# Kernel optimization log

Measured on AMD Instinct MI355X. Metric: run time of the kernel, lower is better.

The kernel has to match this reference:

```python
import jax, jax.numpy as jnp
import numpy as np
import math

DIM = 1024
NUM_HEADS = 16
HEAD_DIM = DIM // NUM_HEADS
EPS = 1e-6
DILATED = 2
WINDOW = 2  # window_size init arg; actual window = L * WINDOW per side


def setup_inputs() -> dict:
    key = jax.random.key(0)
    ks = jax.random.split(key, 14)
    B, S = 1, 8704
    x = jax.random.normal(ks[0], (B, S, DIM), jnp.float32)
    ang = jax.random.uniform(ks[1], (S, HEAD_DIM // 2), jnp.float32, -jnp.pi, jnp.pi)
    freqs_cos = jnp.cos(ang)
    freqs_sin = jnp.sin(ang)
    def lin(k):
        return 0.02 * jax.random.normal(k, (DIM, DIM), jnp.float32)
    def bias(k):
        return 0.01 * jax.random.normal(k, (DIM,), jnp.float32)
    return {
        'x': x, 'freqs_cos': freqs_cos, 'freqs_sin': freqs_sin,
        'wq': lin(ks[2]), 'bq': bias(ks[3]),
        'wk': lin(ks[4]), 'bk': bias(ks[5]),
        'wv': lin(ks[6]), 'bv': bias(ks[7]),
        'wo': lin(ks[8]), 'bo': bias(ks[9]),
        'gq': 1.0 + 0.02 * jax.random.normal(ks[10], (DIM,), jnp.float32),
        'gk': 1.0 + 0.02 * jax.random.normal(ks[11], (DIM,), jnp.float32),
        'f': 34, 'L': 256,
    }


def rmsnorm(h, g):
    return h * jax.lax.rsqrt(jnp.mean(h * h, axis=-1, keepdims=True) + EPS) * g


def rope(h, cos, sin):
    # h: [B,S,D] viewed as interleaved complex pairs per head, rotated by unit freqs
    B, S, D = h.shape
    hp = h.reshape(B, S, NUM_HEADS, HEAD_DIM // 2, 2)
    a, b = hp[..., 0], hp[..., 1]
    c = cos[None, :, None, :]
    s = sin[None, :, None, :]
    ra = a * c - b * s
    rb = a * s + b * c
    return jnp.stack([ra, rb], axis=-1).reshape(B, S, D)


def windowed_attention(q, k, v, w):
    # sliding-window attention: query i attends keys j with |i-j| <= w (inclusive)
    B, S, D = q.shape
    H, hd = NUM_HEADS, HEAD_DIM
    def heads(t):
        return t.reshape(B, S, H, hd).transpose(0, 2, 1, 3)  # [B,H,S,hd]
    qh, kh, vh = heads(q), heads(k), heads(v)
    C = w  # block size == window -> only 3 neighbor key blocks per query block
    pad = (-S) % C
    Sp = S + pad
    nb = Sp // C
    def blocks(t):
        return jnp.pad(t, ((0, 0), (0, 0), (0, pad), (0, 0))).reshape(B, H, nb, C, hd)
    qb = blocks(qh)
    def win(t):
        tb = jnp.pad(blocks(t), ((0, 0), (0, 0), (1, 1), (0, 0), (0, 0)))
        return jnp.concatenate([tb[:, :, i:i + nb] for i in range(3)], axis=3)  # [B,H,nb,3C,hd]
    kw_, vw_ = win(kh), win(vh)
    scores = jnp.einsum('bhnqd,bhnkd->bhnqk', qb, kw_) * (1.0 / math.sqrt(hd))
    qi = jnp.arange(nb)[:, None, None] * C + jnp.arange(C)[None, :, None]      # [nb,C,1]
    kj = (jnp.arange(nb)[:, None, None] - 1) * C + jnp.arange(3 * C)[None, None, :]  # [nb,1,3C]
    valid = (kj >= 0) & (kj < S) & (qi - kj <= w) & (kj - qi <= w)
    scores = jnp.where(valid, scores, -1e9)
    p = jax.nn.softmax(scores, axis=-1)
    o = jnp.einsum('bhnqk,bhnkd->bhnqd', p, vw_)
    return o.reshape(B, H, Sp, hd)[:, :, :S].transpose(0, 2, 1, 3).reshape(B, S, D)


def reference(x, freqs_cos, freqs_sin, wq, bq, wk, bk, wv, bv, wo, bo, gq, gk, f, L):
    B, S, D = x.shape
    q = rope(rmsnorm(x @ wq + bq, gq), freqs_cos, freqs_sin)
    k = rope(rmsnorm(x @ wk + bk, gk), freqs_cos, freqs_sin)
    v = x @ wv + bv
    w = L * WINDOW
    use_dilated = DILATED > 1 and S // (DILATED * L) > 1
    if use_dilated:
        blk = DILATED * L
        pad_len = blk - S % blk  # == blk when S % blk == 0 (faithful to torch code)
        Sp = S + pad_len
        n = Sp // blk
        def padd(t):
            return jnp.pad(t, ((0, 0), (0, pad_len), (0, 0)))
        def dil(t):
            # 'b (n d l) c -> (b d) (n l) c'
            return t.reshape(B, n, DILATED, L, D).transpose(0, 2, 1, 3, 4).reshape(B * DILATED, n * L, D)
        q, k, v = dil(padd(q)), dil(padd(k)), dil(padd(v))
    o = windowed_attention(q, k, v, w)
    out = o @ wo + bo
    if use_dilated:
        # '(b d) (n l) c -> b (n d l) c', then drop pad
        out = out.reshape(B, DILATED, n, L, D).transpose(0, 2, 1, 3, 4).reshape(B, n * DILATED * L, D)
        out = out[:, :S]
    return out
```

## Files before the change

kernel.cpp:

```cpp
#include <hip/hip_runtime.h>
#include <hip/hip_bf16.h>
#include <stdint.h>

#define DIM 1024
#define NH 16
#define HD 64
#define S_ORIG 8704
#define WIN 512

typedef __attribute__((ext_vector_type(8))) short short8;
typedef __attribute__((ext_vector_type(4))) float f32x4;

__device__ __forceinline__ float bf2f(unsigned short u) {
    return __uint_as_float(((unsigned int)u) << 16);
}
__device__ __forceinline__ unsigned short f2bf(float f) {
    unsigned int x = __float_as_uint(f);
    unsigned int r = x + 0x7fffu + ((x >> 16) & 1u);
    return (unsigned short)(r >> 16);
}
__device__ __forceinline__ unsigned int pkbf(float a, float b) {
    unsigned int ua = (__float_as_uint(a) + 0x8000u) >> 16;
    unsigned int ub = (__float_as_uint(b) + 0x8000u) & 0xffff0000u;
    return ua | ub;
}

#define GLD_LDS(gptr, lptr) \
    __builtin_amdgcn_global_load_lds((const __attribute__((address_space(1))) void*)(gptr), \
                                     (__attribute__((address_space(3))) void*)(lptr), 16, 0, 0)

__global__ __launch_bounds__(256) void cvt_x(const float* __restrict__ x,
                                             unsigned short* __restrict__ xb) {
    int i = (blockIdx.x * 256 + threadIdx.x) * 4;
    float4 v = *(const float4*)(x + i);
    ushort4 o;
    o.x = f2bf(v.x); o.y = f2bf(v.y); o.z = f2bf(v.z); o.w = f2bf(v.w);
    *(ushort4*)(xb + i) = o;
}

__global__ __launch_bounds__(256) void transpose_w(const float* __restrict__ w0,
                                                   const float* __restrict__ w1,
                                                   const float* __restrict__ w2,
                                                   const float* __restrict__ w3,
                                                   unsigned short* __restrict__ wt) {
    __shared__ float ts[64][65];
    const int z = blockIdx.z;
    const float* w = z == 0 ? w0 : z == 1 ? w1 : z == 2 ? w2 : w3;
    unsigned short* o = wt + (size_t)z * DIM * DIM;
    const int kb = blockIdx.x * 64, nb = blockIdx.y * 64;
    const int t = threadIdx.x, c = t & 63, r4 = t >> 6;
#pragma unroll
    for (int rr = 0; rr < 16; rr++) {
        int row = rr * 4 + r4;
        ts[row][c] = w[(size_t)(kb + row) * DIM + nb + c];
    }
    __syncthreads();
#pragma unroll
    for (int rr = 0; rr < 16; rr++) {
        int nl = rr * 4 + r4;
        o[(size_t)(nb + nl) * DIM + kb + c] = f2bf(ts[c][nl]);
    }
}

template <int OUTF32>
__global__ __launch_bounds__(256) void gemm_bf16(const unsigned short* __restrict__ A,
                                                 const unsigned short* __restrict__ Bt,
                                                 const float* __restrict__ b0,
                                                 const float* __restrict__ b1,
                                                 const float* __restrict__ b2,
                                                 void* __restrict__ Cout) {
    __shared__ __align__(16) unsigned short As[128 * 32];
    __shared__ __align__(16) unsigned short Bs[128 * 32];
    const int z = blockIdx.z;
    const unsigned short* B = Bt + (size_t)z * DIM * DIM;
    const float* bias = z == 0 ? b0 : (z == 1 ? b1 : b2);
    const int m0 = blockIdx.y * 128, n0 = blockIdx.x * 128;
    const int tid = threadIdx.x;
    const int lane = tid & 63, wv = tid >> 6;
    const int wr = wv >> 1, wc = wv & 1;
    const int quad = lane >> 4, r = lane & 15;

    f32x4 acc[4][4];
#pragma unroll
    for (int i = 0; i < 4; i++)
#pragma unroll
        for (int j = 0; j < 4; j++)
#pragma unroll
            for (int t4 = 0; t4 < 4; t4++) acc[i][j][t4] = 0.0f;

    const unsigned short* a_base = A + (size_t)m0 * DIM;
    const unsigned short* b_base = B + (size_t)n0 * DIM;
    const int c0 = wv * 128 + lane;
    const int r0 = c0 >> 2, o0 = (c0 & 3) * 8;
    const int c1 = c0 + 64;
    const int r1 = c1 >> 2, o1 = (c1 & 3) * 8;
    unsigned short* lA0 = &As[(size_t)(wv * 128) * 8];
    unsigned short* lA1 = &As[(size_t)(wv * 128 + 64) * 8];
    unsigned short* lB0 = &Bs[(size_t)(wv * 128) * 8];
    unsigned short* lB1 = &Bs[(size_t)(wv * 128 + 64) * 8];

    for (int k0 = 0; k0 < DIM; k0 += 32) {
        __syncthreads();
        GLD_LDS(a_base + (size_t)r0 * DIM + k0 + o0, lA0);
        GLD_LDS(a_base + (size_t)r1 * DIM + k0 + o1, lA1);
        GLD_LDS(b_base + (size_t)r0 * DIM + k0 + o0, lB0);
        GLD_LDS(b_base + (size_t)r1 * DIM + k0 + o1, lB1);
        __syncthreads();
        short8 af[4], bfr[4];
#pragma unroll
        for (int i = 0; i < 4; i++)
            af[i] = *(const short8*)&As[(wr * 64 + i * 16 + r) * 32 + quad * 8];
#pragma unroll
        for (int j = 0; j < 4; j++)
            bfr[j] = *(const short8*)&Bs[(wc * 64 + j * 16 + r) * 32 + quad * 8];
#pragma unroll
        for (int i = 0; i < 4; i++)
#pragma unroll
            for (int j = 0; j < 4; j++)
                acc[i][j] = __builtin_amdgcn_mfma_f32_16x16x32_bf16(af[i], bfr[j], acc[i][j], 0, 0, 0);
    }

#pragma unroll
    for (int i = 0; i < 4; i++) {
        const int row = m0 + wr * 64 + i * 16 + quad * 4;
#pragma unroll
        for (int j = 0; j < 4; j++) {
            const int col = n0 + wc * 64 + j * 16 + r;
            const float bvl = bias[col];
#pragma unroll
            for (int t4 = 0; t4 < 4; t4++) {
                float vv = acc[i][j][t4] + bvl;
                if (OUTF32) {
                    ((float*)Cout)[(size_t)(row + t4) * DIM + col] = vv;
                } else {
                    ((unsigned short*)Cout)[(size_t)z * S_ORIG * DIM + (size_t)(row + t4) * DIM + col] = f2bf(vv);
                }
            }
        }
    }
}

__global__ __launch_bounds__(256) void norm_rope(unsigned short* __restrict__ hq,
                                                 unsigned short* __restrict__ hk,
                                                 const float* __restrict__ gq,
                                                 const float* __restrict__ gk,
                                                 const float* __restrict__ fcos,
                                                 const float* __restrict__ fsin) {
    const int srow = blockIdx.x;
    const int z = blockIdx.y;
    unsigned short* h = z == 0 ? hq : hk;
    const float* g = z == 0 ? gq : gk;
    const int tid = threadIdx.x;
    const int base = tid * 4;
    unsigned short* hp = h + (size_t)srow * DIM;

    ushort4 raw = *(const ushort4*)(hp + base);
    float v0 = bf2f(raw.x), v1 = bf2f(raw.y), v2 = bf2f(raw.z), v3 = bf2f(raw.w);
    float ss = v0 * v0 + v1 * v1 + v2 * v2 + v3 * v3;
#pragma unroll
    for (int off = 1; off < 64; off <<= 1) ss += __shfl_xor(ss, off, 64);
    __shared__ float red[4];
    if ((tid & 63) == 0) red[tid >> 6] = ss;
    __syncthreads();
    ss = red[0] + red[1] + red[2] + red[3];
    const float rinv = rsqrtf(ss * (1.0f / DIM) + 1e-6f);

    float4 gv = *(const float4*)(g + base);
    v0 *= rinv * gv.x;
    v1 *= rinv * gv.y;
    v2 *= rinv * gv.z;
    v3 *= rinv * gv.w;

    const int i0 = (base & 63) >> 1;
    float2 cs = *(const float2*)(fcos + (size_t)srow * 32 + i0);
    float2 sn = *(const float2*)(fsin + (size_t)srow * 32 + i0);
    float ra0 = v0 * cs.x - v1 * sn.x;
    float rb0 = v0 * sn.x + v1 * cs.x;
    float ra1 = v2 * cs.y - v3 * sn.y;
    float rb1 = v2 * sn.y + v3 * cs.y;
    ushort4 o;
    o.x = f2bf(ra0); o.y = f2bf(rb0); o.z = f2bf(ra1); o.w = f2bf(rb1);
    *(ushort4*)(hp + base) = o;
}

__global__ __launch_bounds__(256) void attn(const unsigned short* __restrict__ qkv,
                                            unsigned short* __restrict__ ob) {
    __shared__ __align__(16) unsigned short Ks[64 * 72];
    __shared__ __align__(16) unsigned short Vt[64 * 72];
    __shared__ __align__(16) unsigned short Ps[4][16 * 72];

    const int head = blockIdx.x >> 1;
    const int d = blockIdx.x & 1;
    const int qt = blockIdx.y;
    const int tid = threadIdx.x;
    const int lane = tid & 63, wv = tid >> 6;
    const int quad = lane >> 4, r16 = lane & 15;

    const unsigned short* qb = qkv;
    const unsigned short* kb = qkv + (size_t)S_ORIG * DIM;
    const unsigned short* vb = qkv + (size_t)2 * S_ORIG * DIM;

    const int qi = qt * 64 + wv * 16 + r16;
    const int og_q = ((qi >> 8) << 9) + d * 256 + (qi & 255);
    short8 qf[2];
    {
        const unsigned short* qrow = qb + (size_t)og_q * DIM + head * HD + quad * 8;
#pragma unroll
        for (int c = 0; c < 2; c++) {
            union { int4 i4; unsigned short u[8]; short8 s8; } in, outv;
            in.i4 = *(const int4*)(qrow + c * 32);
#pragma unroll
            for (int j = 0; j < 8; j++) outv.u[j] = f2bf(bf2f(in.u[j]) * 0.125f);
            qf[c] = outv.s8;
        }
    }

    f32x4 oacc[4];
    float lsum = 0.0f;
#pragma unroll
    for (int nt = 0; nt < 4; nt++)
#pragma unroll
        for (int rr = 0; rr < 4; rr++) oacc[nt][rr] = 0.0f;

    const int kt_lo = (qt - 8 > 0) ? (qt - 8) : 0;
    const int kt_hi = (qt + 8 < 67) ? (qt + 8) : 67;

    const int st_row0 = tid >> 3, st_ch = (tid & 7) * 8;
    const int vt_kk = (tid & 31) * 2, vt_d0 = (tid >> 5) * 8;

    for (int kt = kt_lo; kt <= kt_hi; kt++) {
        const int kbase = kt * 64;
        __syncthreads();

#pragma unroll
        for (int half = 0; half < 2; half++) {
            const int row = st_row0 + half * 32;
            const int kj = kbase + row;
            const int ok = ((kj >> 8) << 9) + d * 256 + (kj & 255);
            *(int4*)&Ks[row * 72 + st_ch] = *(const int4*)(kb + (size_t)ok * DIM + head * HD + st_ch);
        }
        {
            const int kj0 = kbase + vt_kk;
            const int ok0 = ((kj0 >> 8) << 9) + d * 256 + (kj0 & 255);
            union { int4 i4; unsigned short u[8]; } a0, a1;
            a0.i4 = *(const int4*)(vb + (size_t)ok0 * DIM + head * HD + vt_d0);
            a1.i4 = *(const int4*)(vb + (size_t)(ok0 + 1) * DIM + head * HD + vt_d0);
#pragma unroll
            for (int i = 0; i < 8; i++) {
                unsigned int pack = (unsigned int)a0.u[i] | ((unsigned int)a1.u[i] << 16);
                *(unsigned int*)&Vt[(vt_d0 + i) * 72 + vt_kk] = pack;
            }
        }
        __syncthreads();

        f32x4 sv[4];
#pragma unroll
        for (int nt = 0; nt < 4; nt++) {
            short8 k0f = *(const short8*)&Ks[(nt * 16 + r16) * 72 + quad * 8];
            short8 k1f = *(const short8*)&Ks[(nt * 16 + r16) * 72 + 32 + quad * 8];
            f32x4 a = {0.0f, 0.0f, 0.0f, 0.0f};
            a = __builtin_amdgcn_mfma_f32_16x16x32_bf16(k0f, qf[0], a, 0, 0, 0);
            a = __builtin_amdgcn_mfma_f32_16x16x32_bf16(k1f, qf[1], a, 0, 0, 0);
            sv[nt] = a;
        }

        const bool edge = (kt == qt - 8) || (kt == qt + 8);
        unsigned short* pw = &Ps[wv][0];
#pragma unroll
        for (int nt = 0; nt < 4; nt++) {
            float p[4];
#pragma unroll
            for (int rr = 0; rr < 4; rr++) {
                float e = __expf(sv[nt][rr]);
                if (edge) {
                    const int kj = kbase + nt * 16 + quad * 4 + rr;
                    const int dl = qi - kj;
                    if (dl > WIN || dl < -WIN) e = 0.0f;
                }
                p[rr] = e;
            }
            lsum += (p[0] + p[1]) + (p[2] + p[3]);
            uint2 pk;
            pk.x = pkbf(p[0], p[1]);
            pk.y = pkbf(p[2], p[3]);
            *(uint2*)&pw[r16 * 72 + nt * 16 + quad * 4] = pk;
        }
        __asm__ volatile("s_waitcnt lgkmcnt(0)" ::: "memory");

        short8 pf0 = *(const short8*)&pw[r16 * 72 + quad * 8];
        short8 pf1 = *(const short8*)&pw[r16 * 72 + 32 + quad * 8];
#pragma unroll
        for (int nt = 0; nt < 4; nt++) {
            short8 v0f = *(const short8*)&Vt[(nt * 16 + r16) * 72 + quad * 8];
            short8 v1f = *(const short8*)&Vt[(nt * 16 + r16) * 72 + 32 + quad * 8];
            oacc[nt] = __builtin_amdgcn_mfma_f32_16x16x32_bf16(v0f, pf0, oacc[nt], 0, 0, 0);
            oacc[nt] = __builtin_amdgcn_mfma_f32_16x16x32_bf16(v1f, pf1, oacc[nt], 0, 0, 0);
        }
    }

    lsum += __shfl_xor(lsum, 16, 64);
    lsum += __shfl_xor(lsum, 32, 64);
    {
        const int cnt = (qi + WIN < 4607 ? qi + WIN : 4607) - 4351;
        if (cnt > 0) lsum += (float)cnt;
    }
    const float linv = 1.0f / lsum;

#pragma unroll
    for (int nt = 0; nt < 4; nt++) {
        ushort4 o;
        o.x = f2bf(oacc[nt][0] * linv);
        o.y = f2bf(oacc[nt][1] * linv);
        o.z = f2bf(oacc[nt][2] * linv);
        o.w = f2bf(oacc[nt][3] * linv);
        *(ushort4*)&ob[(size_t)og_q * DIM + head * HD + nt * 16 + quad * 4] = o;
    }
}

extern "C" void kernel_launch(void* const* d_in, const int* in_sizes, int n_in,
                              void* d_out, int out_size, void* d_ws, size_t ws_size,
                              hipStream_t stream) {
    const float* x    = (const float*)d_in[0];
    const float* fcos = (const float*)d_in[1];
    const float* fsin = (const float*)d_in[2];
    const float* wq   = (const float*)d_in[3];
    const float* bq   = (const float*)d_in[4];
    const float* wk   = (const float*)d_in[5];
    const float* bk   = (const float*)d_in[6];
    const float* wv   = (const float*)d_in[7];
    const float* bv   = (const float*)d_in[8];
    const float* wo   = (const float*)d_in[9];
    const float* bo   = (const float*)d_in[10];
    const float* gq   = (const float*)d_in[11];
    const float* gk   = (const float*)d_in[12];

    char* ws = (char*)d_ws;
    unsigned short* xb = (unsigned short*)(ws);
    unsigned short* wt = (unsigned short*)(ws + 17825792);
    unsigned short* h  = (unsigned short*)(ws + 26214400);
    unsigned short* ob = (unsigned short*)(ws + 79691776);
    float* outp = (float*)d_out;

    cvt_x<<<8704, 256, 0, stream>>>(x, xb);
    transpose_w<<<dim3(16, 16, 4), 256, 0, stream>>>(wq, wk, wv, wo, wt);
    gemm_bf16<0><<<dim3(8, 68, 3), 256, 0, stream>>>(xb, wt, bq, bk, bv, (void*)h);
    norm_rope<<<dim3(8704, 2), 256, 0, stream>>>(h, h + (size_t)S_ORIG * DIM, gq, gk, fcos, fsin);
    attn<<<dim3(32, 68), 256, 0, stream>>>(h, ob);
    gemm_bf16<1><<<dim3(8, 68, 1), 256, 0, stream>>>(ob, wt + (size_t)3 * DIM * DIM, bo, bo, bo, (void*)outp);
}
```

Baseline: 334.0 us.

## Process two query tiles per attention block to reuse staged K/V tiles

Each attention workgroup now handles two adjacent 64-row query tiles, loading each K/V tile into shared memory once and applying it to both query tiles. This roughly halves global K/V loads and the number of K/V staging passes, and halves the grid. The exponent is switched to exp2f, with the log2(e) factor folded into the query scale. The trade-offs are higher register pressure from the doubled accumulators and K/V fragments held in registers, and fewer workgroups to fill the GPU.

```diff
diff --git a/kernel.cpp b/kernel.cpp
--- a/kernel.cpp
+++ b/kernel.cpp
@@ -191,7 +191,7 @@
 
     const int head = blockIdx.x >> 1;
     const int d = blockIdx.x & 1;
-    const int qt = blockIdx.y;
+    const int qt0 = blockIdx.y * 2;
     const int tid = threadIdx.x;
     const int lane = tid & 63, wv = tid >> 6;
     const int quad = lane >> 4, r16 = lane & 15;
@@ -200,30 +200,34 @@
     const unsigned short* kb = qkv + (size_t)S_ORIG * DIM;
     const unsigned short* vb = qkv + (size_t)2 * S_ORIG * DIM;
 
-    const int qi = qt * 64 + wv * 16 + r16;
-    const int og_q = ((qi >> 8) << 9) + d * 256 + (qi & 255);
-    short8 qf[2];
-    {
-        const unsigned short* qrow = qb + (size_t)og_q * DIM + head * HD + quad * 8;
+    int qi[2], og_q[2];
+    short8 qf[2][2];
+#pragma unroll
+    for (int t = 0; t < 2; t++) {
+        qi[t] = (qt0 + t) * 64 + wv * 16 + r16;
+        og_q[t] = ((qi[t] >> 8) << 9) + d * 256 + (qi[t] & 255);
+        const unsigned short* qrow = qb + (size_t)og_q[t] * DIM + head * HD + quad * 8;
 #pragma unroll
         for (int c = 0; c < 2; c++) {
             union { int4 i4; unsigned short u[8]; short8 s8; } in, outv;
             in.i4 = *(const int4*)(qrow + c * 32);
 #pragma unroll
-            for (int j = 0; j < 8; j++) outv.u[j] = f2bf(bf2f(in.u[j]) * 0.125f);
-            qf[c] = outv.s8;
-        }
-    }
-
-    f32x4 oacc[4];
-    float lsum = 0.0f;
-#pragma unroll
-    for (int nt = 0; nt < 4; nt++)
-#pragma unroll
-        for (int rr = 0; rr < 4; rr++) oacc[nt][rr] = 0.0f;
-
-    const int kt_lo = (qt - 8 > 0) ? (qt - 8) : 0;
-    const int kt_hi = (qt + 8 < 67) ? (qt + 8) : 67;
+            for (int j = 0; j < 8; j++) outv.u[j] = f2bf(bf2f(in.u[j]) * 0.18033688f);
+            qf[t][c] = outv.s8;
+        }
+    }
+
+    f32x4 oacc[2][4];
+    float lsum[2] = {0.0f, 0.0f};
+#pragma unroll
+    for (int t = 0; t < 2; t++)
+#pragma unroll
+        for (int nt = 0; nt < 4; nt++)
+#pragma unroll
+            for (int rr = 0; rr < 4; rr++) oacc[t][nt][rr] = 0.0f;
+
+    const int kt_lo = (qt0 - 8 > 0) ? (qt0 - 8) : 0;
+    const int kt_hi = (qt0 + 9 < 67) ? (qt0 + 9) : 67;
 
     const int st_row0 = tid >> 3, st_ch = (tid & 7) * 8;
     const int vt_kk = (tid & 31) * 2, vt_d0 = (tid >> 5) * 8;
@@ -253,67 +257,80 @@
         }
         __syncthreads();
 
-        f32x4 sv[4];
+        short8 kf[4][2], vf[4][2];
 #pragma unroll
         for (int nt = 0; nt < 4; nt++) {
-            short8 k0f = *(const short8*)&Ks[(nt * 16 + r16) * 72 + quad * 8];
-            short8 k1f = *(const short8*)&Ks[(nt * 16 + r16) * 72 + 32 + quad * 8];
-            f32x4 a = {0.0f, 0.0f, 0.0f, 0.0f};
-            a = __builtin_amdgcn_mfma_f32_16x16x32_bf16(k0f, qf[0], a, 0, 0, 0);
-            a = __builtin_amdgcn_mfma_f32_16x16x32_bf16(k1f, qf[1], a, 0, 0, 0);
-            sv[nt] = a;
-        }
-
-        const bool edge = (kt == qt - 8) || (kt == qt + 8);
+            kf[nt][0] = *(const short8*)&Ks[(nt * 16 + r16) * 72 + quad * 8];
+            kf[nt][1] = *(const short8*)&Ks[(nt * 16 + r16) * 72 + 32 + quad * 8];
+            vf[nt][0] = *(const short8*)&Vt[(nt * 16 + r16) * 72 + quad * 8];
+            vf[nt][1] = *(const short8*)&Vt[(nt * 16 + r16) * 72 + 32 + quad * 8];
+        }
+
         unsigned short* pw = &Ps[wv][0];
 #pragma unroll
+        for (int t = 0; t < 2; t++) {
+            const int qtl = qt0 + t;
+            if (kt < qtl - 8 || kt > qtl + 8) continue;
+
+            f32x4 sv[4];
+#pragma unroll
+            for (int nt = 0; nt < 4; nt++) {
+                f32x4 a = {0.0f, 0.0f, 0.0f, 0.0f};
+                a = __builtin_amdgcn_mfma_f32_16x16x32_bf16(kf[nt][0], qf[t][0], a, 0, 0, 0);
+                a = __builtin_amdgcn_mfma_f32_16x16x32_bf16(kf[nt][1], qf[t][1], a, 0, 0, 0);
+                sv[nt] = a;
+            }
+
+            const bool edge = (kt == qtl - 8) || (kt == qtl + 8);
+            __asm__ volatile("s_waitcnt lgkmcnt(0)" ::: "memory");
+#pragma unroll
+            for (int nt = 0; nt < 4; nt++) {
+                float p[4];
+#pragma unroll
+                for (int rr = 0; rr < 4; rr++) {
+                    float e = exp2f(sv[nt][rr]);
+                    if (edge) {
+                        const int kj = kbase + nt * 16 + quad * 4 + rr;
+                        const int dl = qi[t] - kj;
+                        if (dl > WIN || dl < -WIN) e = 0.0f;
+                    }
+                    p[rr] = e;
+                }
+                lsum[t] += (p[0] + p[1]) + (p[2] + p[3]);
+                uint2 pk;
+                pk.x = pkbf(p[0], p[1]);
+                pk.y = pkbf(p[2], p[3]);
+                *(uint2*)&pw[r16 * 72 + nt * 16 + quad * 4] = pk;
+            }
+            __asm__ volatile("s_waitcnt lgkmcnt(0)" ::: "memory");
+
+            short8 pf0 = *(const short8*)&pw[r16 * 72 + quad * 8];
+            short8 pf1 = *(const short8*)&pw[r16 * 72 + 32 + quad * 8];
+#pragma unroll
+            for (int nt = 0; nt < 4; nt++) {
+                oacc[t][nt] = __builtin_amdgcn_mfma_f32_16x16x32_bf16(vf[nt][0], pf0, oacc[t][nt], 0, 0, 0);
+                oacc[t][nt] = __builtin_amdgcn_mfma_f32_16x16x32_bf16(vf[nt][1], pf1, oacc[t][nt], 0, 0, 0);
+            }
+        }
+    }
+
+#pragma unroll
+    for (int t = 0; t < 2; t++) {
+        float ls = lsum[t];
+        ls += __shfl_xor(ls, 16, 64);
+        ls += __shfl_xor(ls, 32, 64);
+        const int cnt = (qi[t] + WIN < 4607 ? qi[t] + WIN : 4607) - 4351;
+        if (cnt > 0) ls += (float)cnt;
+        const float linv = 1.0f / ls;
+#pragma unroll
         for (int nt = 0; nt < 4; nt++) {
-            float p[4];
-#pragma unroll
-            for (int rr = 0; rr < 4; rr++) {
-                float e = __expf(sv[nt][rr]);
-                if (edge) {
-                    const int kj = kbase + nt * 16 + quad * 4 + rr;
-                    const int dl = qi - kj;
-                    if (dl > WIN || dl < -WIN) e = 0.0f;
-                }
-                p[rr] = e;
-            }
-            lsum += (p[0] + p[1]) + (p[2] + p[3]);
-            uint2 pk;
-            pk.x = pkbf(p[0], p[1]);
-            pk.y = pkbf(p[2], p[3]);
-            *(uint2*)&pw[r16 * 72 + nt * 16 + quad * 4] = pk;
-        }
-        __asm__ volatile("s_waitcnt lgkmcnt(0)" ::: "memory");
-
-        short8 pf0 = *(const short8*)&pw[r16 * 72 + quad * 8];
-        short8 pf1 = *(const short8*)&pw[r16 * 72 + 32 + quad * 8];
-#pragma unroll
-        for (int nt = 0; nt < 4; nt++) {
-            short8 v0f = *(const short8*)&Vt[(nt * 16 + r16) * 72 + quad * 8];
-            short8 v1f = *(const short8*)&Vt[(nt * 16 + r16) * 72 + 32 + quad * 8];
-            oacc[nt] = __builtin_amdgcn_mfma_f32_16x16x32_bf16(v0f, pf0, oacc[nt], 0, 0, 0);
-            oacc[nt] = __builtin_amdgcn_mfma_f32_16x16x32_bf16(v1f, pf1, oacc[nt], 0, 0, 0);
-        }
-    }
-
-    lsum += __shfl_xor(lsum, 16, 64);
-    lsum += __shfl_xor(lsum, 32, 64);
-    {
-        const int cnt = (qi + WIN < 4607 ? qi + WIN : 4607) - 4351;
-        if (cnt > 0) lsum += (float)cnt;
-    }
-    const float linv = 1.0f / lsum;
-
-#pragma unroll
-    for (int nt = 0; nt < 4; nt++) {
-        ushort4 o;
-        o.x = f2bf(oacc[nt][0] * linv);
-        o.y = f2bf(oacc[nt][1] * linv);
-        o.z = f2bf(oacc[nt][2] * linv);
-        o.w = f2bf(oacc[nt][3] * linv);
-        *(ushort4*)&ob[(size_t)og_q * DIM + head * HD + nt * 16 + quad * 4] = o;
+            ushort4 o;
+            o.x = f2bf(oacc[t][nt][0] * linv);
+            o.y = f2bf(oacc[t][nt][1] * linv);
+            o.z = f2bf(oacc[t][nt][2] * linv);
+            o.w = f2bf(oacc[t][nt][3] * linv);
+            *(ushort4*)&ob[(size_t)og_q[t] * DIM + head * HD + nt * 16 + quad * 4] = o;
+        }
     }
 }
 
@@ -345,6 +362,6 @@
     transpose_w<<<dim3(16, 16, 4), 256, 0, stream>>>(wq, wk, wv, wo, wt);
     gemm_bf16<0><<<dim3(8, 68, 3), 256, 0, stream>>>(xb, wt, bq, bk, bv, (void*)h);
     norm_rope<<<dim3(8704, 2), 256, 0, stream>>>(h, h + (size_t)S_ORIG * DIM, gq, gk, fcos, fsin);
-    attn<<<dim3(32, 68), 256, 0, stream>>>(h, ob);
+    attn<<<dim3(32, 34), 256, 0, stream>>>(h, ob);
     gemm_bf16<1><<<dim3(8, 68, 1), 256, 0, stream>>>(ob, wt + (size_t)3 * DIM * DIM, bo, bo, bo, (void*)outp);
 }
```

New measurement: 354.4 us. 1.06x slower.
